# Kernel tuning notes

Hardware: AMD Instinct MI355X
Metric: run time of the kernel (lower is better)

## Reference

```python
import jax, jax.numpy as jnp
import numpy as np

BATCH, SIZE_IN, SIZE_OUT = 2048, 256, 512


def setup_inputs() -> dict:
    key = jax.random.key(0)
    kx, ka = jax.random.split(key)
    x = jax.random.normal(kx, (BATCH, SIZE_IN), dtype=jnp.float32)
    A = jax.random.normal(ka, (SIZE_IN, SIZE_OUT), dtype=jnp.float32)
    return {"x": x, "A": A}


def reference(x, A):
    # W = sigmoid(A): [size_in, size_out]
    W = jax.nn.sigmoid(A)
    # tropical (max-times) matmul: out[i,k] = max_j W[j,k] * x[i,j]
    # broadcast [B,1,J_in->axis1]... x: [B,J,1], W: [1,J,K] -> [B,J,K] -> max over J
    out = jnp.max(x[:, :, None] * W[None, :, :], axis=1)  # [B, K]
    return out
```

## Files before the change

kernel.cpp:

```cpp
#include <hip/hip_runtime.h>


typedef _Float16 h1;
typedef __attribute__((ext_vector_type(2))) _Float16 h2v;
typedef __attribute__((ext_vector_type(4))) float f4;
typedef __attribute__((ext_vector_type(4))) unsigned int u4;
typedef __attribute__((ext_vector_type(8))) unsigned int u8;

constexpr int JD = 256;
constexpr int KD = 512;

__device__ __forceinline__ float sigmoidf_fast(float a) {
    return 1.0f / (1.0f + __expf(-a));
}

__device__ __forceinline__ h2v asH2(unsigned int u) {
    union { unsigned int x; h2v h; } c; c.x = u; return c.h;
}

__global__ __launch_bounds__(256) void prepack(const float* __restrict__ x,
                                               const float* __restrict__ A,
                                               u4* __restrict__ Wq,
                                               u4* __restrict__ xp4) {
    const int b = (int)blockIdx.x;
    if (b < 64) {
        const int t  = b * 256 + (int)threadIdx.x;
        const int p4 = t >> 9;
        const int k  = t & 511;
        union { u4 v; h2v h[4]; } u;
        #pragma unroll
        for (int q = 0; q < 4; ++q) {
            const float a0 = A[(8 * p4 + 2 * q) * KD + k];
            const float a1 = A[(8 * p4 + 2 * q + 1) * KD + k];
            u.h[q] = h2v{(h1)sigmoidf_fast(a0), (h1)sigmoidf_fast(a1)};
        }
        Wq[p4 * 512 + k] = u.v;
    } else {
        const int g = (b - 64) * 256 + (int)threadIdx.x;
        const f4 x0 = *(const f4*)&x[g * 8];
        const f4 x1 = *(const f4*)&x[g * 8 + 4];
        union { u4 v; h2v h[4]; } u;
        u.h[0] = h2v{(h1)x0.x, (h1)x0.y};
        u.h[1] = h2v{(h1)x0.z, (h1)x0.w};
        u.h[2] = h2v{(h1)x1.x, (h1)x1.y};
        u.h[3] = h2v{(h1)x1.z, (h1)x1.w};
        xp4[g] = u.v;
    }
}

__global__ __launch_bounds__(256) void tropical_main(
        const unsigned int* __restrict__ xp,
        const u4* __restrict__ Wq,
        float* __restrict__ out) {
    __shared__ u4 Wl[32 * 64];

    const int t    = (int)threadIdx.x;
    const int lane = t & 63;
    const int wv   = __builtin_amdgcn_readfirstlane(t >> 6);
    const int kg   = (int)blockIdx.x & 7;
    const int rg   = (int)blockIdx.x >> 3;
    const int k0   = kg * 64;
    const int r0   = rg * 16 + wv * 4;

    #pragma unroll
    for (int i = 0; i < 8; ++i) {
        const int p4 = wv * 8 + i;
        Wl[p4 * 64 + lane] = Wq[p4 * 512 + k0 + lane];
    }
    __syncthreads();

    const unsigned int* xr = xp + r0 * 128;

    h2v acc[4];
    #pragma unroll
    for (int r = 0; r < 4; ++r)
        acc[r] = h2v{(h1)(-65504.0f), (h1)(-65504.0f)};

    #pragma unroll 2
    for (int c = 0; c < 16; ++c) {
        u8 X[4];
        #pragma unroll
        for (int r = 0; r < 4; ++r)
            X[r] = *(const u8*)(xr + r * 128 + c * 8);

        union { u4 v; h2v h[4]; } w0, w1;
        w0.v = Wl[(2 * c + 0) * 64 + lane];
        w1.v = Wl[(2 * c + 1) * 64 + lane];

        #pragma unroll
        for (int r = 0; r < 4; ++r) {
            #pragma unroll
            for (int q = 0; q < 4; ++q) {
                acc[r] = __builtin_elementwise_max(acc[r],
                                                   asH2(X[r][q]) * w0.h[q]);
                acc[r] = __builtin_elementwise_max(acc[r],
                                                   asH2(X[r][4 + q]) * w1.h[q]);
            }
        }
    }

    const int k = k0 + lane;
    #pragma unroll
    for (int r = 0; r < 4; ++r)
        out[(r0 + r) * KD + k] = fmaxf((float)acc[r][0], (float)acc[r][1]);
}

extern "C" void kernel_launch(void* const* d_in, const int* in_sizes, int n_in,
                              void* d_out, int out_size, void* d_ws, size_t ws_size,
                              hipStream_t stream) {
    const float* x = (const float*)d_in[0];
    const float* A = (const float*)d_in[1];
    float* out = (float*)d_out;

    u4* Wq  = (u4*)d_ws;
    u4* xp4 = (u4*)((char*)d_ws + 256 * 1024);

    hipLaunchKernelGGL(prepack, dim3(320), dim3(256), 0, stream, x, A, Wq, xp4);

    hipLaunchKernelGGL(tropical_main, dim3(1024), dim3(256), 0, stream,
                       (const unsigned int*)xp4, Wq, out);
}
```

Baseline: 21.70 us.

## Fuse prepack into main kernel with scalar x loads and double-buffered inline asm

Removes the separate prepack launch. Each block now converts its own 16 rows of x to fp16 into workspace, and computes sigmoid(A) for its 64 output columns directly into shared memory. The main loop reads the fp16 x rows through scalar loads (s_load_dwordx8) and the weights through ds_read_b128, double-buffered, with hand-written packed fp16 mul/max in inline asm. The aim is to drop one kernel launch and its global round trip. In exchange, every block recomputes the sigmoid of A for its column slice (about 128x redundant work overall) and reads fp32 A from L2 instead of packed fp16.

New measurement: 27.73 us. +27.7%, slower.

```diff
diff --git a/kernel.cpp b/kernel.cpp
--- a/kernel.cpp
+++ b/kernel.cpp
@@ -14,44 +14,11 @@
     return 1.0f / (1.0f + __expf(-a));
 }
 
-__device__ __forceinline__ h2v asH2(unsigned int u) {
-    union { unsigned int x; h2v h; } c; c.x = u; return c.h;
-}
-
-__global__ __launch_bounds__(256) void prepack(const float* __restrict__ x,
-                                               const float* __restrict__ A,
-                                               u4* __restrict__ Wq,
-                                               u4* __restrict__ xp4) {
-    const int b = (int)blockIdx.x;
-    if (b < 64) {
-        const int t  = b * 256 + (int)threadIdx.x;
-        const int p4 = t >> 9;
-        const int k  = t & 511;
-        union { u4 v; h2v h[4]; } u;
-        #pragma unroll
-        for (int q = 0; q < 4; ++q) {
-            const float a0 = A[(8 * p4 + 2 * q) * KD + k];
-            const float a1 = A[(8 * p4 + 2 * q + 1) * KD + k];
-            u.h[q] = h2v{(h1)sigmoidf_fast(a0), (h1)sigmoidf_fast(a1)};
-        }
-        Wq[p4 * 512 + k] = u.v;
-    } else {
-        const int g = (b - 64) * 256 + (int)threadIdx.x;
-        const f4 x0 = *(const f4*)&x[g * 8];
-        const f4 x1 = *(const f4*)&x[g * 8 + 4];
-        union { u4 v; h2v h[4]; } u;
-        u.h[0] = h2v{(h1)x0.x, (h1)x0.y};
-        u.h[1] = h2v{(h1)x0.z, (h1)x0.w};
-        u.h[2] = h2v{(h1)x1.x, (h1)x1.y};
-        u.h[3] = h2v{(h1)x1.z, (h1)x1.w};
-        xp4[g] = u.v;
-    }
-}
-
-__global__ __launch_bounds__(256) void tropical_main(
-        const unsigned int* __restrict__ xp,
-        const u4* __restrict__ Wq,
-        float* __restrict__ out) {
+__global__ __launch_bounds__(256) void tropical_one(
+        const float* __restrict__ x,
+        const float* __restrict__ A,
+        float* __restrict__ out,
+        unsigned int* ws) {
     __shared__ u4 Wl[32 * 64];
 
     const int t    = (int)threadIdx.x;
@@ -60,49 +27,110 @@
     const int kg   = (int)blockIdx.x & 7;
     const int rg   = (int)blockIdx.x >> 3;
     const int k0   = kg * 64;
-    const int r0   = rg * 16 + wv * 4;
+    const int i0   = rg * 16;
 
-    #pragma unroll
-    for (int i = 0; i < 8; ++i) {
-        const int p4 = wv * 8 + i;
-        Wl[p4 * 64 + lane] = Wq[p4 * 512 + k0 + lane];
+    {
+        const int row = t >> 4;
+        const int cb  = (t & 15) * 16;
+        const float* xs = x + (i0 + row) * JD + cb;
+        f4 v0 = ((const f4*)xs)[0];
+        f4 v1 = ((const f4*)xs)[1];
+        f4 v2 = ((const f4*)xs)[2];
+        f4 v3 = ((const f4*)xs)[3];
+        union { u4 v; h2v h[4]; } a, b;
+        a.h[0] = h2v{(h1)v0.x, (h1)v0.y};
+        a.h[1] = h2v{(h1)v0.z, (h1)v0.w};
+        a.h[2] = h2v{(h1)v1.x, (h1)v1.y};
+        a.h[3] = h2v{(h1)v1.z, (h1)v1.w};
+        b.h[0] = h2v{(h1)v2.x, (h1)v2.y};
+        b.h[1] = h2v{(h1)v2.z, (h1)v2.w};
+        b.h[2] = h2v{(h1)v3.x, (h1)v3.y};
+        b.h[3] = h2v{(h1)v3.z, (h1)v3.w};
+        unsigned int* dst = ws + rg * 2048 + row * 128 + (t & 15) * 8;
+        *(u4*)dst       = a.v;
+        *(u4*)(dst + 4) = b.v;
+    }
+    asm volatile("s_waitcnt vmcnt(0)" ::: "memory");
+
+    {
+        const int grp = t >> 6;
+        const float* Ak = A + k0 + lane;
+        #pragma unroll 2
+        for (int pass = 0; pass < 8; ++pass) {
+            const int p4 = grp * 8 + pass;
+            union { u4 v; h2v h[4]; } u;
+            #pragma unroll
+            for (int q = 0; q < 4; ++q) {
+                const float a0 = Ak[(8 * p4 + 2 * q) * KD];
+                const float a1 = Ak[(8 * p4 + 2 * q + 1) * KD];
+                u.h[q] = h2v{(h1)sigmoidf_fast(a0), (h1)sigmoidf_fast(a1)};
+            }
+            Wl[p4 * 64 + lane] = u.v;
+        }
     }
     __syncthreads();
 
-    const unsigned int* xr = xp + r0 * 128;
+    const unsigned int* xrow = ws + rg * 2048 + wv * 4 * 128;
+    const unsigned int voffb =
+        (unsigned int)(unsigned long long)(&Wl[0]) + (unsigned int)lane * 16u;
 
-    h2v acc[4];
-    #pragma unroll
-    for (int r = 0; r < 4; ++r)
-        acc[r] = h2v{(h1)(-65504.0f), (h1)(-65504.0f)};
+    unsigned int acc[4] = {0xFBFFFBFFu, 0xFBFFFBFFu, 0xFBFFFBFFu, 0xFBFFFBFFu};
 
-    #pragma unroll 2
-    for (int c = 0; c < 16; ++c) {
-        u8 X[4];
-        #pragma unroll
-        for (int r = 0; r < 4; ++r)
-            X[r] = *(const u8*)(xr + r * 128 + c * 8);
+    u8 X[2][4];
+    u4 W[2][2];
 
-        union { u4 v; h2v h[4]; } w0, w1;
-        w0.v = Wl[(2 * c + 0) * 64 + lane];
-        w1.v = Wl[(2 * c + 1) * 64 + lane];
-
+    auto issue = [&](int buf, int c) {
+        const unsigned int* p = xrow + c * 8;
+        asm volatile("s_load_dwordx8 %0, %1, 0x0" : "=s"(X[buf][0]) : "s"(p));
+        asm volatile("s_load_dwordx8 %0, %1, 0x0" : "=s"(X[buf][1]) : "s"(p + 128));
+        asm volatile("s_load_dwordx8 %0, %1, 0x0" : "=s"(X[buf][2]) : "s"(p + 256));
+        asm volatile("s_load_dwordx8 %0, %1, 0x0" : "=s"(X[buf][3]) : "s"(p + 384));
+        const unsigned int vo = voffb + (unsigned int)c * 2048u;
+        asm volatile("ds_read_b128 %0, %1" : "=v"(W[buf][0]) : "v"(vo));
+        asm volatile("ds_read_b128 %0, %1" : "=v"(W[buf][1]) : "v"(vo + 1024u));
+    };
+    auto wait = [&](int buf) {
+        asm volatile("s_waitcnt lgkmcnt(0)"
+                     : "+s"(X[buf][0]), "+s"(X[buf][1]),
+                       "+s"(X[buf][2]), "+s"(X[buf][3]),
+                       "+v"(W[buf][0]), "+v"(W[buf][1]));
+    };
+    auto compute = [&](int buf) {
+        union { u4 v; unsigned int d[4]; } w0, w1;
+        w0.v = W[buf][0];
+        w1.v = W[buf][1];
         #pragma unroll
         for (int r = 0; r < 4; ++r) {
             #pragma unroll
             for (int q = 0; q < 4; ++q) {
-                acc[r] = __builtin_elementwise_max(acc[r],
-                                                   asH2(X[r][q]) * w0.h[q]);
-                acc[r] = __builtin_elementwise_max(acc[r],
-                                                   asH2(X[r][4 + q]) * w1.h[q]);
+                unsigned int p0, p1;
+                asm("v_pk_mul_f16 %0, %1, %2"
+                    : "=v"(p0) : "s"(X[buf][r][q]), "v"(w0.d[q]));
+                asm("v_pk_max_f16 %0, %1, %0" : "+v"(acc[r]) : "v"(p0));
+                asm("v_pk_mul_f16 %0, %1, %2"
+                    : "=v"(p1) : "s"(X[buf][r][4 + q]), "v"(w1.d[q]));
+                asm("v_pk_max_f16 %0, %1, %0" : "+v"(acc[r]) : "v"(p1));
             }
         }
+    };
+
+    issue(0, 0);
+    wait(0);
+    #pragma unroll
+    for (int c = 0; c < 16; ++c) {
+        const int cur = c & 1, nxt = cur ^ 1;
+        if (c + 1 < 16) issue(nxt, c + 1);
+        compute(cur);
+        if (c + 1 < 16) wait(nxt);
     }
 
-    const int k = k0 + lane;
     #pragma unroll
-    for (int r = 0; r < 4; ++r)
-        out[(r0 + r) * KD + k] = fmaxf((float)acc[r][0], (float)acc[r][1]);
+    for (int r = 0; r < 4; ++r) {
+        union { unsigned int u; h2v h; } cv;
+        cv.u = acc[r];
+        out[(i0 + wv * 4 + r) * KD + k0 + lane] =
+            fmaxf((float)cv.h[0], (float)cv.h[1]);
+    }
 }
 
 extern "C" void kernel_launch(void* const* d_in, const int* in_sizes, int n_in,
@@ -111,12 +139,8 @@
     const float* x = (const float*)d_in[0];
     const float* A = (const float*)d_in[1];
     float* out = (float*)d_out;
+    unsigned int* ws = (unsigned int*)d_ws;
 
-    u4* Wq  = (u4*)d_ws;
-    u4* xp4 = (u4*)((char*)d_ws + 256 * 1024);
-
-    hipLaunchKernelGGL(prepack, dim3(320), dim3(256), 0, stream, x, A, Wq, xp4);
-
-    hipLaunchKernelGGL(tropical_main, dim3(1024), dim3(256), 0, stream,
-                       (const unsigned int*)xp4, Wq, out);
+    hipLaunchKernelGGL(tropical_one, dim3(1024), dim3(256), 0, stream,
+                       x, A, out, ws);
 }
```

## Fuse prepack into main kernel, computing sigmoid per block and using fp32 x

Applied to the files above, without the earlier changes.

Removes the separate prepack launch. Each block now computes sigmoid(A) for its 64-column slice straight into shared memory as fp16, and reads x directly in fp32. The max-product accumulation moves from packed fp16 to scalar fp32 math. This saves a kernel launch and a workspace round trip, but every row-group block repeats the sigmoid work, reads twice as many x bytes, and loses the packed-fp16 throughput.

After: 27.66 us. 1.27x slower.

```diff
diff --git a/kernel.cpp b/kernel.cpp
--- a/kernel.cpp
+++ b/kernel.cpp
@@ -4,8 +4,8 @@
 typedef _Float16 h1;
 typedef __attribute__((ext_vector_type(2))) _Float16 h2v;
 typedef __attribute__((ext_vector_type(4))) float f4;
+typedef __attribute__((ext_vector_type(8))) float f8;
 typedef __attribute__((ext_vector_type(4))) unsigned int u4;
-typedef __attribute__((ext_vector_type(8))) unsigned int u8;
 
 constexpr int JD = 256;
 constexpr int KD = 512;
@@ -14,43 +14,9 @@
     return 1.0f / (1.0f + __expf(-a));
 }
 
-__device__ __forceinline__ h2v asH2(unsigned int u) {
-    union { unsigned int x; h2v h; } c; c.x = u; return c.h;
-}
-
-__global__ __launch_bounds__(256) void prepack(const float* __restrict__ x,
-                                               const float* __restrict__ A,
-                                               u4* __restrict__ Wq,
-                                               u4* __restrict__ xp4) {
-    const int b = (int)blockIdx.x;
-    if (b < 64) {
-        const int t  = b * 256 + (int)threadIdx.x;
-        const int p4 = t >> 9;
-        const int k  = t & 511;
-        union { u4 v; h2v h[4]; } u;
-        #pragma unroll
-        for (int q = 0; q < 4; ++q) {
-            const float a0 = A[(8 * p4 + 2 * q) * KD + k];
-            const float a1 = A[(8 * p4 + 2 * q + 1) * KD + k];
-            u.h[q] = h2v{(h1)sigmoidf_fast(a0), (h1)sigmoidf_fast(a1)};
-        }
-        Wq[p4 * 512 + k] = u.v;
-    } else {
-        const int g = (b - 64) * 256 + (int)threadIdx.x;
-        const f4 x0 = *(const f4*)&x[g * 8];
-        const f4 x1 = *(const f4*)&x[g * 8 + 4];
-        union { u4 v; h2v h[4]; } u;
-        u.h[0] = h2v{(h1)x0.x, (h1)x0.y};
-        u.h[1] = h2v{(h1)x0.z, (h1)x0.w};
-        u.h[2] = h2v{(h1)x1.x, (h1)x1.y};
-        u.h[3] = h2v{(h1)x1.z, (h1)x1.w};
-        xp4[g] = u.v;
-    }
-}
-
-__global__ __launch_bounds__(256) void tropical_main(
-        const unsigned int* __restrict__ xp,
-        const u4* __restrict__ Wq,
+__global__ __launch_bounds__(256) void tropical_one(
+        const float* __restrict__ x,
+        const float* __restrict__ A,
         float* __restrict__ out) {
     __shared__ u4 Wl[32 * 64];
 
@@ -60,49 +26,63 @@
     const int kg   = (int)blockIdx.x & 7;
     const int rg   = (int)blockIdx.x >> 3;
     const int k0   = kg * 64;
-    const int r0   = rg * 16 + wv * 4;
+    const int i0   = rg * 16;
 
-    #pragma unroll
-    for (int i = 0; i < 8; ++i) {
-        const int p4 = wv * 8 + i;
-        Wl[p4 * 64 + lane] = Wq[p4 * 512 + k0 + lane];
+    {
+        const float* Ak = A + k0 + lane;
+        const int c0 = (t >> 6) * 8;
+        #pragma unroll 2
+        for (int cc = 0; cc < 8; ++cc) {
+            const int c = c0 + cc;
+            union { u4 v; h2v h[4]; } u;
+            #pragma unroll
+            for (int q = 0; q < 4; ++q) {
+                const float a0 = Ak[(8 * c + 2 * q) * KD];
+                const float a1 = Ak[(8 * c + 2 * q + 1) * KD];
+                u.h[q] = h2v{(h1)sigmoidf_fast(a0), (h1)sigmoidf_fast(a1)};
+            }
+            Wl[c * 64 + lane] = u.v;
+        }
     }
     __syncthreads();
 
-    const unsigned int* xr = xp + r0 * 128;
+    const float* xr = x + (i0 + wv * 4) * JD;
 
-    h2v acc[4];
+    float acc[4];
     #pragma unroll
-    for (int r = 0; r < 4; ++r)
-        acc[r] = h2v{(h1)(-65504.0f), (h1)(-65504.0f)};
+    for (int r = 0; r < 4; ++r) acc[r] = -__builtin_inff();
 
     #pragma unroll 2
-    for (int c = 0; c < 16; ++c) {
-        u8 X[4];
+    for (int c = 0; c < 32; ++c) {
+        f8 X[4];
         #pragma unroll
         for (int r = 0; r < 4; ++r)
-            X[r] = *(const u8*)(xr + r * 128 + c * 8);
+            X[r] = *(const f8*)(xr + r * JD + c * 8);
 
-        union { u4 v; h2v h[4]; } w0, w1;
-        w0.v = Wl[(2 * c + 0) * 64 + lane];
-        w1.v = Wl[(2 * c + 1) * 64 + lane];
+        union { u4 v; h2v h[4]; } w;
+        w.v = Wl[c * 64 + lane];
+
+        float wf[8];
+        #pragma unroll
+        for (int q = 0; q < 4; ++q) {
+            wf[2 * q]     = (float)w.h[q][0];
+            wf[2 * q + 1] = (float)w.h[q][1];
+        }
 
         #pragma unroll
         for (int r = 0; r < 4; ++r) {
             #pragma unroll
             for (int q = 0; q < 4; ++q) {
-                acc[r] = __builtin_elementwise_max(acc[r],
-                                                   asH2(X[r][q]) * w0.h[q]);
-                acc[r] = __builtin_elementwise_max(acc[r],
-                                                   asH2(X[r][4 + q]) * w1.h[q]);
+                acc[r] = fmaxf(fmaxf(X[r][2 * q] * wf[2 * q],
+                                     X[r][2 * q + 1] * wf[2 * q + 1]),
+                               acc[r]);
             }
         }
     }
 
-    const int k = k0 + lane;
     #pragma unroll
     for (int r = 0; r < 4; ++r)
-        out[(r0 + r) * KD + k] = fmaxf((float)acc[r][0], (float)acc[r][1]);
+        out[(i0 + wv * 4 + r) * KD + k0 + lane] = acc[r];
 }
 
 extern "C" void kernel_launch(void* const* d_in, const int* in_sizes, int n_in,
@@ -112,11 +92,6 @@
     const float* A = (const float*)d_in[1];
     float* out = (float*)d_out;
 
-    u4* Wq  = (u4*)d_ws;
-    u4* xp4 = (u4*)((char*)d_ws + 256 * 1024);
-
-    hipLaunchKernelGGL(prepack, dim3(320), dim3(256), 0, stream, x, A, Wq, xp4);
-
-    hipLaunchKernelGGL(tropical_main, dim3(1024), dim3(256), 0, stream,
-                       (const unsigned int*)xp4, Wq, out);
+    hipLaunchKernelGGL(tropical_one, dim3(1024), dim3(256), 0, stream,
+                       x, A, out);
 }
```
